# Kernel tuning notes

Measured on AMD Instinct MI355X. Metric: run time of the kernel, lower is better.

## Reference

```python
import jax, jax.numpy as jnp
import numpy as np

N = 25000      # nodes
E = 400000     # edges
D = 128        # num_hidden (per-head out dim)
H = 3          # heads
NEG_SLOPE = 0.2
BN_EPS = 1e-5


def _gatv2(x, edge_index, Wl, bl, Wr, br, att, bias):
    """PyG GATv2Conv (concat=True, add_self_loops=True, dropout=0).
    x: [N, Din]; Wl/Wr: [Din, H*D]; att: [H, D]; bias: [H*D].
    """
    n = x.shape[0]
    h, d = att.shape
    loops = jnp.arange(n)
    src = jnp.concatenate([edge_index[0], loops])  # [E+N]
    dst = jnp.concatenate([edge_index[1], loops])
    xl = (x @ Wl + bl).reshape(n, h, d)  # source transform
    xr = (x @ Wr + br).reshape(n, h, d)  # target transform
    # edge scores: a^T LeakyReLU(xl_j + xr_i)
    e = jax.nn.leaky_relu(xl[src] + xr[dst], NEG_SLOPE)   # [E+N, H, D]
    score = jnp.einsum('ehd,hd->eh', e, att)              # [E+N, H]
    # segment softmax over incoming edges of each dst node
    m = jax.ops.segment_max(score, dst, num_segments=n)   # [N, H]
    ex = jnp.exp(score - m[dst])
    denom = jax.ops.segment_sum(ex, dst, num_segments=n)  # [N, H]
    alpha = ex / denom[dst]                               # [E+N, H]
    out = jax.ops.segment_sum(alpha[:, :, None] * xl[src], dst, num_segments=n)
    return out.reshape(n, h * d) + bias                   # [N, H*D]


def _batchnorm(x, gamma, beta):
    mu = jnp.mean(x, axis=0)
    var = jnp.var(x, axis=0)  # biased, as torch BN uses for normalization
    return gamma * (x - mu) * jax.lax.rsqrt(var + BN_EPS) + beta


def setup_inputs() -> dict:
    key = jax.random.key(0)
    ks = iter(jax.random.split(key, 32))
    s = 0.1
    p = {}
    p['x'] = jax.random.normal(next(ks), (N, D), jnp.float32)
    p['edge_index'] = jax.random.randint(next(ks), (2, E), 0, N, jnp.int64)
    for i in (1, 2):
        p[f'Wl{i}'] = s * jax.random.normal(next(ks), (D, H * D), jnp.float32)
        p[f'bl{i}'] = jnp.zeros((H * D,), jnp.float32)
        p[f'Wr{i}'] = s * jax.random.normal(next(ks), (D, H * D), jnp.float32)
        p[f'br{i}'] = jnp.zeros((H * D,), jnp.float32)
        p[f'att{i}'] = s * jax.random.normal(next(ks), (H, D), jnp.float32)
        p[f'bc{i}'] = jnp.zeros((H * D,), jnp.float32)
        p[f'g{i}'] = jnp.ones((D,), jnp.float32)
        p[f'be{i}'] = jnp.zeros((D,), jnp.float32)
    p['W1'] = s * jax.random.normal(next(ks), (H * D, D), jnp.float32)
    p['b1'] = jnp.zeros((D,), jnp.float32)
    p['W2'] = s * jax.random.normal(next(ks), (2 * H * D, D), jnp.float32)
    p['b2'] = jnp.zeros((D,), jnp.float32)
    return p


def reference(x, edge_index, Wl1, bl1, Wr1, br1, att1, bc1, g1, be1,
              Wl2, bl2, Wr2, br2, att2, bc2, g2, be2, W1, b1, W2, b2):
    x_in = _gatv2(x, edge_index, Wl1, bl1, Wr1, br1, att1, bc1)  # [N, H*D]
    h = _batchnorm(x_in @ W1 + b1, g1, be1)
    h = jax.nn.relu(h)                                           # [N, D]
    h2 = _gatv2(h, edge_index, Wl2, bl2, Wr2, br2, att2, bc2)    # [N, H*D]
    out = jnp.concatenate([h2, x_in], axis=1) @ W2 + b2          # [N, D]
    out = _batchnorm(out, g2, be2)
    return jax.nn.relu(out)
```

## Files before the change

kernel.cpp:

```cpp
#include <hip/hip_runtime.h>
#include <math.h>

#define NN 25000
#define NE 400000
#define DD 128
#define HD 384
#define NEG 0.2f
#define EPS 1e-5f

typedef unsigned int u32;
typedef unsigned short u16;
typedef __attribute__((ext_vector_type(8))) short short8;
typedef __attribute__((ext_vector_type(4))) float floatx4;
typedef __attribute__((ext_vector_type(2))) float f32x2;

__device__ __forceinline__ u32 bf16_1(float x) {
    u32 u = __float_as_uint(x);
    return (u + 0x7fffu + ((u >> 16) & 1u)) >> 16;
}
__device__ __forceinline__ float blo(u32 u) { return __uint_as_float(u << 16); }
__device__ __forceinline__ float bhi(u32 u) { return __uint_as_float(u & 0xffff0000u); }

__device__ __forceinline__ void up8f2(uint4 u, f32x2* f) {
    f[0] = f32x2{blo(u.x), bhi(u.x)};
    f[1] = f32x2{blo(u.y), bhi(u.y)};
    f[2] = f32x2{blo(u.z), bhi(u.z)};
    f[3] = f32x2{blo(u.w), bhi(u.w)};
}

__device__ __forceinline__ f32x2 pk_add(f32x2 a, f32x2 b) {
    f32x2 d; asm("v_pk_add_f32 %0, %1, %2" : "=v"(d) : "v"(a), "v"(b)); return d;
}
__device__ __forceinline__ f32x2 pk_fma(f32x2 a, f32x2 b, f32x2 c) {
    f32x2 d; asm("v_pk_fma_f32 %0, %1, %2, %3" : "=v"(d) : "v"(a), "v"(b), "v"(c)); return d;
}
__device__ __forceinline__ f32x2 fabs2(f32x2 v) {
    u32 a = __float_as_uint(v.x) & 0x7fffffffu;
    u32 b = __float_as_uint(v.y) & 0x7fffffffu;
    return f32x2{__uint_as_float(a), __uint_as_float(b)};
}

__device__ __forceinline__ float row_sum16(float x) {
    int t;
    t = __builtin_amdgcn_update_dpp(0, __float_as_int(x), 0x121, 0xf, 0xf, false);
    x += __int_as_float(t);
    t = __builtin_amdgcn_update_dpp(0, __float_as_int(x), 0x122, 0xf, 0xf, false);
    x += __int_as_float(t);
    t = __builtin_amdgcn_update_dpp(0, __float_as_int(x), 0x124, 0xf, 0xf, false);
    x += __int_as_float(t);
    t = __builtin_amdgcn_update_dpp(0, __float_as_int(x), 0x128, 0xf, 0xf, false);
    x += __int_as_float(t);
    return x;
}

__global__ void k_fill_edges(const int* __restrict__ src, const int* __restrict__ dst,
                             int* __restrict__ cur, int* __restrict__ col_src) {
    int e = blockIdx.x * 256 + threadIdx.x;
    if (e < NE) {
        int d = dst[e];
        int p = atomicAdd(&cur[d], 1);
        col_src[(d << 6) + p] = src[e];
    }
}

__global__ void k_cast_all(const float* __restrict__ x,
                           const float* __restrict__ Wl1, const float* __restrict__ Wr1,
                           const float* __restrict__ W1,
                           const float* __restrict__ Wl2, const float* __restrict__ Wr2,
                           const float* __restrict__ W2,
                           const float* __restrict__ bl1, const float* __restrict__ br1,
                           const float* __restrict__ bl2, const float* __restrict__ br2,
                           const float* __restrict__ att1, const float* __restrict__ att2,
                           u16* __restrict__ xb, u16* __restrict__ WfT1,
                           u16* __restrict__ W1T, u16* __restrict__ WfT2,
                           u16* __restrict__ W2T,
                           float* __restrict__ fb1, float* __restrict__ fb2,
                           float* __restrict__ attc1, float* __restrict__ attc2,
                           float* __restrict__ stats) {
    int i = blockIdx.x * 256 + threadIdx.x;
    if (i < 400000) {
        const float4* xp = (const float4*)(x + (size_t)i * 8);
        float4 a = xp[0], b = xp[1];
        uint4 w;
        w.x = bf16_1(a.x) | (bf16_1(a.y) << 16);
        w.y = bf16_1(a.z) | (bf16_1(a.w) << 16);
        w.z = bf16_1(b.x) | (bf16_1(b.y) << 16);
        w.w = bf16_1(b.z) | (bf16_1(b.w) << 16);
        *(uint4*)(xb + (size_t)i * 8) = w;
        return;
    }
    i -= 400000;
    if (i < 49152) { int k = i / 384, n = i - k * 384; WfT1[n * 128 + k] = (u16)bf16_1(Wl1[i]); return; }
    i -= 49152;
    if (i < 49152) { int k = i / 384, n = i - k * 384; WfT1[(384 + n) * 128 + k] = (u16)bf16_1(Wr1[i]); return; }
    i -= 49152;
    if (i < 49152) { int k = i / 128, n = i - k * 128; W1T[n * 384 + k] = (u16)bf16_1(W1[i]); return; }
    i -= 49152;
    if (i < 49152) { int k = i / 384, n = i - k * 384; WfT2[n * 128 + k] = (u16)bf16_1(Wl2[i]); return; }
    i -= 49152;
    if (i < 49152) { int k = i / 384, n = i - k * 384; WfT2[(384 + n) * 128 + k] = (u16)bf16_1(Wr2[i]); return; }
    i -= 49152;
    if (i < 98304) { int k = i / 128, n = i - k * 128; W2T[n * 768 + k] = (u16)bf16_1(W2[i]); return; }
    i -= 98304;
    if (i < 768) { fb1[i] = (i < 384) ? bl1[i] : br1[i - 384]; return; }
    i -= 768;
    if (i < 768) { fb2[i] = (i < 384) ? bl2[i] : br2[i - 384]; return; }
    i -= 768;
    if (i < 384) { attc1[i] = att1[i] * 0.86561702f; return; }
    i -= 384;
    if (i < 384) { attc2[i] = att2[i] * 0.86561702f; return; }
    i -= 384;
    if (i < 512) stats[i] = 0.f;
}
#define CAST_TOTAL (400000 + 5 * 49152 + 98304 + 1536 + 768 + 512)

__global__ __launch_bounds__(256) void k_gemm_k128(
        const u16* __restrict__ A, const u16* __restrict__ BT,
        const float* __restrict__ bias, u16* __restrict__ Cb, int M) {
    __shared__ short sA[128 * 128];
    __shared__ short sB[128 * 128];
    int tid = threadIdx.x;
    int wv = tid >> 6, lane = tid & 63;
    int quad = lane >> 4, m16 = lane & 15;
    int mb = blockIdx.y * 128, nb = blockIdx.x * 128;

#pragma unroll
    for (int j = 0; j < 8; ++j) {
        int L = j * 256 + tid;
        int r = L >> 4, c8 = (L & 15) ^ (r & 15);
        int gr = mb + r; gr = gr < M ? gr : M - 1;
        __builtin_amdgcn_global_load_lds(
            (const __attribute__((address_space(1))) void*)(A + (size_t)gr * 128 + c8 * 8),
            (__attribute__((address_space(3))) void*)(sA + (size_t)L * 8), 16, 0, 0);
    }
#pragma unroll
    for (int j = 0; j < 8; ++j) {
        int L = j * 256 + tid;
        int r = L >> 4, c8 = (L & 15) ^ (r & 15);
        __builtin_amdgcn_global_load_lds(
            (const __attribute__((address_space(1))) void*)(BT + (size_t)(nb + r) * 128 + c8 * 8),
            (__attribute__((address_space(3))) void*)(sB + (size_t)L * 8), 16, 0, 0);
    }
    __syncthreads();

    floatx4 acc[2][8];
#pragma unroll
    for (int mf = 0; mf < 2; ++mf)
#pragma unroll
        for (int nf = 0; nf < 8; ++nf)
#pragma unroll
            for (int r = 0; r < 4; ++r) acc[mf][nf][r] = 0.f;

#pragma unroll
    for (int ks = 0; ks < 4; ++ks) {
        int slot = (ks * 4 + quad) ^ m16;
        int row0 = wv * 32 + m16, row1 = row0 + 16;
        short8 a0 = *(const short8*)(sA + ((size_t)row0 * 16 + slot) * 8);
        short8 a1 = *(const short8*)(sA + ((size_t)row1 * 16 + slot) * 8);
#pragma unroll
        for (int nf = 0; nf < 8; ++nf) {
            short8 b = *(const short8*)(sB + ((size_t)(nf * 16 + m16) * 16 + slot) * 8);
            acc[0][nf] = __builtin_amdgcn_mfma_f32_16x16x32_bf16(a0, b, acc[0][nf], 0, 0, 0);
            acc[1][nf] = __builtin_amdgcn_mfma_f32_16x16x32_bf16(a1, b, acc[1][nf], 0, 0, 0);
        }
    }
    __syncthreads();

#pragma unroll
    for (int mf = 0; mf < 2; ++mf)
#pragma unroll
        for (int nf = 0; nf < 8; ++nf)
#pragma unroll
            for (int r = 0; r < 4; ++r) {
                int row = wv * 32 + mf * 16 + quad * 4 + r;
                int col = nf * 16 + m16;
                sA[row * 128 + col] = (short)bf16_1(acc[mf][nf][r] + bias[nb + col]);
            }
    __syncthreads();
    int xr = nb >= 384;
    int h = (xr ? (nb - 384) : nb) >> 7;
    u16* cb = Cb + ((size_t)(xr * 3 + h) * NN) * 128;
#pragma unroll
    for (int i = 0; i < 8; ++i) {
        int u = i * 256 + tid;
        int row = u >> 4, c8 = u & 15;
        int grow = mb + row;
        if (grow < M)
            *(uint4*)(cb + (size_t)grow * 128 + c8 * 8) = *(const uint4*)(sA + (size_t)u * 8);
    }
}

__global__ __launch_bounds__(256) void k_gemm_bf(
        const u16* __restrict__ A, const u16* __restrict__ BT,
        const float* __restrict__ bias,
        float* __restrict__ Cf, float* __restrict__ stats,
        int M, int N, int K, int lda) {
    __shared__ short smem[17408];
    short* sA = smem;
    short* sB = smem + 8192;
    int tid = threadIdx.x;
    int wv = tid >> 6, lane = tid & 63;
    int quad = lane >> 4, m16 = lane & 15;
    int mb = blockIdx.y * 64, nb = blockIdx.x * 64;

    floatx4 acc[4];
#pragma unroll
    for (int nf = 0; nf < 4; ++nf)
#pragma unroll
        for (int r = 0; r < 4; ++r) acc[nf][r] = 0.f;

    for (int k0 = 0; k0 < K; k0 += 128) {
#pragma unroll
        for (int j = 0; j < 4; ++j) {
            int L = j * 256 + tid;
            int r = L >> 4, c8 = (L & 15) ^ (r & 15);
            int gr = mb + r; gr = gr < M ? gr : M - 1;
            __builtin_amdgcn_global_load_lds(
                (const __attribute__((address_space(1))) void*)(A + (size_t)gr * lda + k0 + c8 * 8),
                (__attribute__((address_space(3))) void*)(sA + (size_t)L * 8), 16, 0, 0);
        }
#pragma unroll
        for (int j = 0; j < 4; ++j) {
            int L = j * 256 + tid;
            int r = L >> 4, c8 = (L & 15) ^ (r & 15);
            __builtin_amdgcn_global_load_lds(
                (const __attribute__((address_space(1))) void*)(BT + (size_t)(nb + r) * K + k0 + c8 * 8),
                (__attribute__((address_space(3))) void*)(sB + (size_t)L * 8), 16, 0, 0);
        }
        __syncthreads();
#pragma unroll
        for (int ks = 0; ks < 4; ++ks) {
            int slot = (ks * 4 + quad) ^ m16;
            short8 a0 = *(const short8*)(sA + ((size_t)(wv * 16 + m16) * 16 + slot) * 8);
#pragma unroll
            for (int nf = 0; nf < 4; ++nf) {
                short8 b = *(const short8*)(sB + ((size_t)(nf * 16 + m16) * 16 + slot) * 8);
                acc[nf] = __builtin_amdgcn_mfma_f32_16x16x32_bf16(a0, b, acc[nf], 0, 0, 0);
            }
        }
        __syncthreads();
    }
    float* fs = (float*)smem;
#pragma unroll
    for (int nf = 0; nf < 4; ++nf)
#pragma unroll
        for (int r = 0; r < 4; ++r) {
            int row = wv * 16 + quad * 4 + r;
            int col = nf * 16 + m16;
            fs[row * 64 + col] = acc[nf][r] + (bias ? bias[nb + col] : 0.f);
        }
    __syncthreads();
#pragma unroll
    for (int i = 0; i < 4; ++i) {
        int u = i * 256 + tid;
        int row = u >> 4, c4 = u & 15;
        int grow = mb + row;
        if (grow < M)
            *(float4*)(Cf + (size_t)grow * N + nb + c4 * 4) = *(const float4*)(fs + (size_t)u * 4);
    }
    if (stats) {
        float* ps = (float*)(smem + 16384);
        int col = tid & 63, qr = tid >> 6;
        int vr = M - mb; vr = vr < 64 ? vr : 64;
        int r0 = qr * 16, r1 = r0 + 16 < vr ? r0 + 16 : vr;
        float s = 0.f, q = 0.f;
        for (int r = r0; r < r1; ++r) { float v = fs[r * 64 + col]; s += v; q += v * v; }
        ps[qr * 64 + col] = s;
        ps[256 + qr * 64 + col] = q;
        __syncthreads();
        if (tid < 64) {
            float ss = ps[tid] + ps[64 + tid] + ps[128 + tid] + ps[192 + tid];
            atomicAdd(&stats[nb + tid], ss);
        } else if (tid < 128) {
            int c = tid - 64;
            float qq = ps[256 + c] + ps[320 + c] + ps[384 + c] + ps[448 + c];
            atomicAdd(&stats[128 + nb + c], qq);
        }
    }
}

__global__ __launch_bounds__(256) void k_gat_h(const u32* __restrict__ XLb,
                                               const u32* __restrict__ XRb,
                                               const float* __restrict__ attc,
                                               const float* __restrict__ bias,
                                               const int* __restrict__ cnt,
                                               const int* __restrict__ col_src,
                                               u32* __restrict__ outb) {
    int h = blockIdx.y;
    const u32* XLh = XLb + (size_t)h * NN * 64;
    const u32* XRh = XRb + (size_t)h * NN * 64;
    int node = blockIdx.x * 4 + (threadIdx.x >> 6);
    int lane = threadIdx.x & 63;
    int g = lane >> 4, gl = lane & 15;

    f32x2 xr2[4], a6[4], acc2[4];
    const f32x2 c23 = {0.66666667f, 0.66666667f};
    up8f2(*(const uint4*)(XRh + (size_t)node * 64 + 4 * gl), xr2);
#pragma unroll
    for (int j = 0; j < 4; ++j) {
        a6[j] = *(const f32x2*)(attc + h * 128 + 8 * gl + 2 * j);
        acc2[j] = f32x2{0.f, 0.f};
    }
    float l = 0.f;

    int e0 = node << 6;
    int cntE = cnt[node];

    int c0i = col_src[e0 + g];
    int c1i = col_src[e0 + g + 4];

    if (g == 0) {
        f32x2 xs[4];
        up8f2(*(const uint4*)(XLh + (size_t)node * 64 + 4 * gl), xs);
        f32x2 p2 = {0.f, 0.f};
#pragma unroll
        for (int j = 0; j < 4; ++j) {
            f32x2 v = pk_add(xs[j], xr2[j]);
            p2 = pk_fma(pk_fma(fabs2(v), c23, v), a6[j], p2);
        }
        float w = __builtin_amdgcn_exp2f(row_sum16(p2.x + p2.y));
        l = w;
        f32x2 w2 = {w, w};
#pragma unroll
        for (int j = 0; j < 4; ++j) acc2[j] = pk_fma(xs[j], w2, acc2[j]);
    }

    uint4 ua = *(const uint4*)(XLh + (size_t)c0i * 64 + 4 * gl);
    uint4 ub = *(const uint4*)(XLh + (size_t)c1i * 64 + 4 * gl);

    for (int t = g; t < cntE; t += 8) {
        uint4 un0 = *(const uint4*)(XLh + (size_t)col_src[e0 + t + 8] * 64 + 4 * gl);
        uint4 un1 = *(const uint4*)(XLh + (size_t)col_src[e0 + t + 12] * 64 + 4 * gl);

        f32x2 xa2[4], xb2[4];
        up8f2(ua, xa2); up8f2(ub, xb2);
        f32x2 pa2 = {0.f, 0.f}, pb2 = {0.f, 0.f};
#pragma unroll
        for (int j = 0; j < 4; ++j) {
            f32x2 va = pk_add(xa2[j], xr2[j]);
            f32x2 vb = pk_add(xb2[j], xr2[j]);
            pa2 = pk_fma(pk_fma(fabs2(va), c23, va), a6[j], pa2);
            pb2 = pk_fma(pk_fma(fabs2(vb), c23, vb), a6[j], pb2);
        }
        float pa = row_sum16(pa2.x + pa2.y);
        float pb = row_sum16(pb2.x + pb2.y);
        float wa = __builtin_amdgcn_exp2f(pa);
        float wb = ((t + 4) < cntE) ? __builtin_amdgcn_exp2f(pb) : 0.f;
        l += wa + wb;
        f32x2 wa2 = {wa, wa}, wb2 = {wb, wb};
#pragma unroll
        for (int j = 0; j < 4; ++j)
            acc2[j] = pk_fma(xa2[j], wa2, pk_fma(xb2[j], wb2, acc2[j]));

        ua = un0; ub = un1;
    }

#pragma unroll
    for (int o = 16; o <= 32; o <<= 1) {
        l += __shfl_xor(l, o);
#pragma unroll
        for (int j = 0; j < 4; ++j) {
            f32x2 s;
            s.x = __shfl_xor(acc2[j].x, o);
            s.y = __shfl_xor(acc2[j].y, o);
            acc2[j] = pk_add(acc2[j], s);
        }
    }

    if (g == 0) {
        float r = 1.f / l;
        float bv[8];
        *(float4*)&bv[0] = *(const float4*)&bias[h * 128 + 8 * gl];
        *(float4*)&bv[4] = *(const float4*)&bias[h * 128 + 8 * gl + 4];
        uint4 w;
        w.x = bf16_1(fmaf(acc2[0].x, r, bv[0])) | (bf16_1(fmaf(acc2[0].y, r, bv[1])) << 16);
        w.y = bf16_1(fmaf(acc2[1].x, r, bv[2])) | (bf16_1(fmaf(acc2[1].y, r, bv[3])) << 16);
        w.z = bf16_1(fmaf(acc2[2].x, r, bv[4])) | (bf16_1(fmaf(acc2[2].y, r, bv[5])) << 16);
        w.w = bf16_1(fmaf(acc2[3].x, r, bv[6])) | (bf16_1(fmaf(acc2[3].y, r, bv[7])) << 16);
        *(uint4*)(outb + (size_t)node * 384 + h * 64 + 4 * gl) = w;
    }
}

__global__ void k_bn_apply(float* __restrict__ y, const float* __restrict__ stats,
                           const float* __restrict__ g, const float* __restrict__ be,
                           u16* __restrict__ yb, int wf) {
    int i = blockIdx.x * 256 + threadIdx.x;
    if (i >= NN * DD / 8) return;
    int idx = i * 8;
    int c0 = idx & 127;
    float v[8];
    *(float4*)&v[0] = *(const float4*)(y + idx);
    *(float4*)&v[4] = *(const float4*)(y + idx + 4);
    const float minv = 1.f / (float)NN;
#pragma unroll
    for (int k = 0; k < 8; ++k) {
        int c = c0 + k;
        float mu = stats[c] * minv;
        float var = stats[128 + c] * minv - mu * mu;
        float sc = g[c] * rsqrtf(var + EPS);
        float sh = be[c] - mu * sc;
        v[k] = fmaxf(fmaf(v[k], sc, sh), 0.f);
    }
    if (wf) {
        *(float4*)(y + idx) = *(const float4*)&v[0];
        *(float4*)(y + idx + 4) = *(const float4*)&v[4];
    }
    if (yb) {
        uint4 w;
        w.x = bf16_1(v[0]) | (bf16_1(v[1]) << 16);
        w.y = bf16_1(v[2]) | (bf16_1(v[3]) << 16);
        w.z = bf16_1(v[4]) | (bf16_1(v[5]) << 16);
        w.w = bf16_1(v[6]) | (bf16_1(v[7]) << 16);
        *(uint4*)(yb + idx) = w;
    }
}


extern "C" void kernel_launch(void* const* d_in, const int* in_sizes, int n_in,
                              void* d_out, int out_size, void* d_ws, size_t ws_size,
                              hipStream_t stream) {
    const float* x    = (const float*)d_in[0];
    const int*   ei   = (const int*)d_in[1];
    const float* Wl1  = (const float*)d_in[2];
    const float* bl1  = (const float*)d_in[3];
    const float* Wr1  = (const float*)d_in[4];
    const float* br1  = (const float*)d_in[5];
    const float* att1 = (const float*)d_in[6];
    const float* bc1  = (const float*)d_in[7];
    const float* g1   = (const float*)d_in[8];
    const float* be1  = (const float*)d_in[9];
    const float* Wl2  = (const float*)d_in[10];
    const float* bl2  = (const float*)d_in[11];
    const float* Wr2  = (const float*)d_in[12];
    const float* br2  = (const float*)d_in[13];
    const float* att2 = (const float*)d_in[14];
    const float* bc2  = (const float*)d_in[15];
    const float* g2   = (const float*)d_in[16];
    const float* be2  = (const float*)d_in[17];
    const float* W1   = (const float*)d_in[18];
    const float* b1   = (const float*)d_in[19];
    const float* W2   = (const float*)d_in[20];
    const float* b2   = (const float*)d_in[21];
    const int* esrc = ei;
    const int* edst = ei + NE;
    float* out = (float*)d_out;

    float* bufD   = (float*)d_ws;
    float* stats  = bufD + 3200000;
    int* cnt      = (int*)(stats + 512);
    int* col_src  = cnt + 25000;
    float* fb1    = (float*)(col_src + 1600024);
    float* fb2    = fb1 + 768;
    float* attc1  = fb2 + 768;
    float* attc2  = attc1 + 384;
    u16* xb       = (u16*)(attc2 + 384);
    u16* XLb      = xb + 3200000;
    u16* XRb      = XLb + 3 * NN * 128;
    u16* bufCat   = XRb + 3 * NN * 128;
    u16* bufDb    = bufCat + 19200000;
    u16* WfT1     = bufDb + 3200000;
    u16* W1T      = WfT1 + 98304;
    u16* WfT2     = W1T + 49152;
    u16* W2T      = WfT2 + 98304;

    hipMemsetAsync(cnt, 0, NN * sizeof(int), stream);
    hipMemsetAsync(col_src, 0, (NN * 64 + 24) * sizeof(int), stream);
    k_cast_all<<<(CAST_TOTAL + 255) / 256, 256, 0, stream>>>(
        x, Wl1, Wr1, W1, Wl2, Wr2, W2, bl1, br1, bl2, br2, att1, att2,
        xb, WfT1, W1T, WfT2, W2T, fb1, fb2, attc1, attc2, stats);
    k_fill_edges<<<(NE + 255) / 256, 256, 0, stream>>>(esrc, edst, cnt, col_src);

    dim3 blk(256);
    dim3 gK(6, (NN + 127) / 128);
    dim3 g64(2, (NN + 63) / 64);
    dim3 gGat((NN + 3) / 4, 3);

    k_gemm_k128<<<gK, blk, 0, stream>>>(xb, WfT1, fb1, XLb, NN);
    k_gat_h<<<gGat, blk, 0, stream>>>((const u32*)XLb, (const u32*)XRb, attc1, bc1,
                                      cnt, col_src, (u32*)bufCat + 192);

    k_gemm_bf<<<g64, blk, 0, stream>>>(bufCat + 384, W1T, b1, bufD, stats, NN, DD, HD, 768);
    k_bn_apply<<<(NN * DD / 8 + 255) / 256, 256, 0, stream>>>(bufD, stats, g1, be1, bufDb, 0);

    k_gemm_k128<<<gK, blk, 0, stream>>>(bufDb, WfT2, fb2, XLb, NN);
    k_gat_h<<<gGat, blk, 0, stream>>>((const u32*)XLb, (const u32*)XRb, attc2, bc2,
                                      cnt, col_src, (u32*)bufCat);

    k_gemm_bf<<<g64, blk, 0, stream>>>(bufCat, W2T, b2, out, stats + 256, NN, DD, 768, 768);
    k_bn_apply<<<(NN * DD / 8 + 255) / 256, 256, 0, stream>>>(out, stats + 256, g2, be2, nullptr, 1);
}
```

Baseline: 342.0 us.

## Fuse edge fill into cast kernel and loop K128 GEMM over all output tiles

The CSR edge-fill kernel is folded into the cast/transpose kernel, which removes one kernel launch. The K=128 GEMM now uses 64-row blocks that load the A tile once and loop over all six 128-column weight tiles, instead of a 2D grid that reloads A for each column tile. This cuts redundant A traffic and the grid size. The trade-off is serialized B tile loads inside each block with extra barriers, and less parallelism per block.

```diff
diff --git a/kernel.cpp b/kernel.cpp
--- a/kernel.cpp
+++ b/kernel.cpp
@@ -53,16 +53,6 @@
     return x;
 }
 
-__global__ void k_fill_edges(const int* __restrict__ src, const int* __restrict__ dst,
-                             int* __restrict__ cur, int* __restrict__ col_src) {
-    int e = blockIdx.x * 256 + threadIdx.x;
-    if (e < NE) {
-        int d = dst[e];
-        int p = atomicAdd(&cur[d], 1);
-        col_src[(d << 6) + p] = src[e];
-    }
-}
-
 __global__ void k_cast_all(const float* __restrict__ x,
                            const float* __restrict__ Wl1, const float* __restrict__ Wr1,
                            const float* __restrict__ W1,
@@ -71,11 +61,13 @@
                            const float* __restrict__ bl1, const float* __restrict__ br1,
                            const float* __restrict__ bl2, const float* __restrict__ br2,
                            const float* __restrict__ att1, const float* __restrict__ att2,
+                           const int* __restrict__ esrc, const int* __restrict__ edst,
                            u16* __restrict__ xb, u16* __restrict__ WfT1,
                            u16* __restrict__ W1T, u16* __restrict__ WfT2,
                            u16* __restrict__ W2T,
                            float* __restrict__ fb1, float* __restrict__ fb2,
                            float* __restrict__ attc1, float* __restrict__ attc2,
+                           int* __restrict__ cnt, int* __restrict__ col_src,
                            float* __restrict__ stats) {
     int i = blockIdx.x * 256 + threadIdx.x;
     if (i < 400000) {
@@ -87,6 +79,13 @@
         w.z = bf16_1(b.x) | (bf16_1(b.y) << 16);
         w.w = bf16_1(b.z) | (bf16_1(b.w) << 16);
         *(uint4*)(xb + (size_t)i * 8) = w;
+        return;
+    }
+    i -= 400000;
+    if (i < 400000) {
+        int d = edst[i];
+        int p = atomicAdd(&cnt[d], 1);
+        col_src[(d << 6) + p] = esrc[i];
         return;
     }
     i -= 400000;
@@ -112,20 +111,20 @@
     i -= 384;
     if (i < 512) stats[i] = 0.f;
 }
-#define CAST_TOTAL (400000 + 5 * 49152 + 98304 + 1536 + 768 + 512)
+#define CAST_TOTAL (400000 + 400000 + 5 * 49152 + 98304 + 1536 + 768 + 512)
 
 __global__ __launch_bounds__(256) void k_gemm_k128(
         const u16* __restrict__ A, const u16* __restrict__ BT,
         const float* __restrict__ bias, u16* __restrict__ Cb, int M) {
-    __shared__ short sA[128 * 128];
+    __shared__ short sA[64 * 128];
     __shared__ short sB[128 * 128];
     int tid = threadIdx.x;
     int wv = tid >> 6, lane = tid & 63;
     int quad = lane >> 4, m16 = lane & 15;
-    int mb = blockIdx.y * 128, nb = blockIdx.x * 128;
-
-#pragma unroll
-    for (int j = 0; j < 8; ++j) {
+    int mb = blockIdx.x * 64;
+
+#pragma unroll
+    for (int j = 0; j < 4; ++j) {
         int L = j * 256 + tid;
         int r = L >> 4, c8 = (L & 15) ^ (r & 15);
         int gr = mb + r; gr = gr < M ? gr : M - 1;
@@ -133,60 +132,59 @@
             (const __attribute__((address_space(1))) void*)(A + (size_t)gr * 128 + c8 * 8),
             (__attribute__((address_space(3))) void*)(sA + (size_t)L * 8), 16, 0, 0);
     }
-#pragma unroll
-    for (int j = 0; j < 8; ++j) {
-        int L = j * 256 + tid;
-        int r = L >> 4, c8 = (L & 15) ^ (r & 15);
-        __builtin_amdgcn_global_load_lds(
-            (const __attribute__((address_space(1))) void*)(BT + (size_t)(nb + r) * 128 + c8 * 8),
-            (__attribute__((address_space(3))) void*)(sB + (size_t)L * 8), 16, 0, 0);
-    }
-    __syncthreads();
-
-    floatx4 acc[2][8];
-#pragma unroll
-    for (int mf = 0; mf < 2; ++mf)
+
+    for (int nb6 = 0; nb6 < 6; ++nb6) {
+        int nb = nb6 * 128;
+        __syncthreads();
+#pragma unroll
+        for (int j = 0; j < 8; ++j) {
+            int L = j * 256 + tid;
+            int r = L >> 4, c8 = (L & 15) ^ (r & 15);
+            __builtin_amdgcn_global_load_lds(
+                (const __attribute__((address_space(1))) void*)(BT + (size_t)(nb + r) * 128 + c8 * 8),
+                (__attribute__((address_space(3))) void*)(sB + (size_t)L * 8), 16, 0, 0);
+        }
+        __syncthreads();
+
+        floatx4 acc[8];
 #pragma unroll
         for (int nf = 0; nf < 8; ++nf)
 #pragma unroll
-            for (int r = 0; r < 4; ++r) acc[mf][nf][r] = 0.f;
-
-#pragma unroll
-    for (int ks = 0; ks < 4; ++ks) {
-        int slot = (ks * 4 + quad) ^ m16;
-        int row0 = wv * 32 + m16, row1 = row0 + 16;
-        short8 a0 = *(const short8*)(sA + ((size_t)row0 * 16 + slot) * 8);
-        short8 a1 = *(const short8*)(sA + ((size_t)row1 * 16 + slot) * 8);
-#pragma unroll
-        for (int nf = 0; nf < 8; ++nf) {
-            short8 b = *(const short8*)(sB + ((size_t)(nf * 16 + m16) * 16 + slot) * 8);
-            acc[0][nf] = __builtin_amdgcn_mfma_f32_16x16x32_bf16(a0, b, acc[0][nf], 0, 0, 0);
-            acc[1][nf] = __builtin_amdgcn_mfma_f32_16x16x32_bf16(a1, b, acc[1][nf], 0, 0, 0);
-        }
-    }
-    __syncthreads();
-
-#pragma unroll
-    for (int mf = 0; mf < 2; ++mf)
+            for (int r = 0; r < 4; ++r) acc[nf][r] = 0.f;
+
+#pragma unroll
+        for (int ks = 0; ks < 4; ++ks) {
+            int slot = (ks * 4 + quad) ^ m16;
+            short8 a0 = *(const short8*)(sA + ((size_t)(wv * 16 + m16) * 16 + slot) * 8);
+#pragma unroll
+            for (int nf = 0; nf < 8; ++nf) {
+                short8 b = *(const short8*)(sB + ((size_t)(nf * 16 + m16) * 16 + slot) * 8);
+                acc[nf] = __builtin_amdgcn_mfma_f32_16x16x32_bf16(a0, b, acc[nf], 0, 0, 0);
+            }
+        }
+        __syncthreads();
+
 #pragma unroll
         for (int nf = 0; nf < 8; ++nf)
 #pragma unroll
             for (int r = 0; r < 4; ++r) {
-                int row = wv * 32 + mf * 16 + quad * 4 + r;
+                int row = wv * 16 + quad * 4 + r;
                 int col = nf * 16 + m16;
-                sA[row * 128 + col] = (short)bf16_1(acc[mf][nf][r] + bias[nb + col]);
+                sB[row * 128 + col] = (short)bf16_1(acc[nf][r] + bias[nb + col]);
             }
-    __syncthreads();
-    int xr = nb >= 384;
-    int h = (xr ? (nb - 384) : nb) >> 7;
-    u16* cb = Cb + ((size_t)(xr * 3 + h) * NN) * 128;
-#pragma unroll
-    for (int i = 0; i < 8; ++i) {
-        int u = i * 256 + tid;
-        int row = u >> 4, c8 = u & 15;
-        int grow = mb + row;
-        if (grow < M)
-            *(uint4*)(cb + (size_t)grow * 128 + c8 * 8) = *(const uint4*)(sA + (size_t)u * 8);
+        __syncthreads();
+
+        int xr = nb >= 384;
+        int h = (xr ? (nb - 384) : nb) >> 7;
+        u16* cb = Cb + ((size_t)(xr * 3 + h) * NN) * 128;
+#pragma unroll
+        for (int i = 0; i < 4; ++i) {
+            int u = i * 256 + tid;
+            int row = u >> 4, c8 = u & 15;
+            int grow = mb + row;
+            if (grow < M)
+                *(uint4*)(cb + (size_t)grow * 128 + c8 * 8) = *(const uint4*)(sB + (size_t)u * 8);
+        }
     }
 }
 
@@ -466,12 +464,11 @@
     hipMemsetAsync(cnt, 0, NN * sizeof(int), stream);
     hipMemsetAsync(col_src, 0, (NN * 64 + 24) * sizeof(int), stream);
     k_cast_all<<<(CAST_TOTAL + 255) / 256, 256, 0, stream>>>(
-        x, Wl1, Wr1, W1, Wl2, Wr2, W2, bl1, br1, bl2, br2, att1, att2,
-        xb, WfT1, W1T, WfT2, W2T, fb1, fb2, attc1, attc2, stats);
-    k_fill_edges<<<(NE + 255) / 256, 256, 0, stream>>>(esrc, edst, cnt, col_src);
+        x, Wl1, Wr1, W1, Wl2, Wr2, W2, bl1, br1, bl2, br2, att1, att2, esrc, edst,
+        xb, WfT1, W1T, WfT2, W2T, fb1, fb2, attc1, attc2, cnt, col_src, stats);
 
     dim3 blk(256);
-    dim3 gK(6, (NN + 127) / 128);
+    dim3 gK((NN + 63) / 64);
     dim3 g64(2, (NN + 63) / 64);
     dim3 gGat((NN + 3) / 4, 3);
 
```

Measured after the change: 338.3 us. Within noise of the previous version (-1.1%).
